# Optimization experiments

Hardware: AMD Instinct MI355X
Metric: run time of the kernel (lower is better)

Reference implementation:

```python
import jax, jax.numpy as jnp
import numpy as np

B, T, C = 2, 2048, 2048
H, KV, D = 16, 4, 128
R = H // KV  # n_rep


def rope_tables(T, D, dtype=jnp.float32):
    half = D // 2
    theta = 1.0 / (10000.0 ** (jnp.arange(half, dtype=jnp.float32) / half))
    pos = jnp.arange(T, dtype=jnp.float32)
    freqs = pos[:, None] * theta[None, :]            # (T, half)
    freqs = jnp.concatenate([freqs, freqs], axis=-1)  # (T, D)
    return jnp.cos(freqs).astype(dtype), jnp.sin(freqs).astype(dtype)


def rotate_half(x):
    half = x.shape[-1] // 2
    return jnp.concatenate([-x[..., half:], x[..., :half]], axis=-1)


def apply_rope(x, cos, sin):
    # x: (B, heads, T, D); cos/sin: (T, D) broadcast over batch/heads
    return x * cos + rotate_half(x) * sin


def setup_inputs() -> dict:
    key = jax.random.key(0)
    kx, kq, kk, kv, ko = jax.random.split(key, 5)
    x = jax.random.normal(kx, (B, T, C), dtype=jnp.float32)
    s = 0.02
    Wq = jax.random.normal(kq, (C, H * D), dtype=jnp.float32) * s
    Wk = jax.random.normal(kk, (C, KV * D), dtype=jnp.float32) * s
    Wv = jax.random.normal(kv, (C, KV * D), dtype=jnp.float32) * s
    Wo = jax.random.normal(ko, (C, C), dtype=jnp.float32) * s
    return {"x": x, "Wq": Wq, "Wk": Wk, "Wv": Wv, "Wo": Wo}


def reference(x, Wq, Wk, Wv, Wo):
    cos, sin = rope_tables(T, D, x.dtype)
    # projections -> (B, heads, T, D)
    q = (x @ Wq).reshape(B, T, H, D).transpose(0, 2, 1, 3)
    k = (x @ Wk).reshape(B, T, KV, D).transpose(0, 2, 1, 3)
    v = (x @ Wv).reshape(B, T, KV, D).transpose(0, 2, 1, 3)
    q = apply_rope(q, cos, sin)
    k = apply_rope(k, cos, sin)
    # GQA: repeat_interleave(n_rep, dim=1) == grouping heads as (KV, R)
    qg = q.reshape(B, KV, R, T, D)
    scale = 1.0 / jnp.sqrt(jnp.asarray(D, dtype=x.dtype))
    scores = jnp.einsum('bgrtd,bgsd->bgrts', qg, k) * scale  # (B,KV,R,T,T)
    causal = jnp.tril(jnp.ones((T, T), dtype=bool))
    scores = jnp.where(causal, scores, jnp.asarray(-jnp.inf, dtype=scores.dtype))
    attn = jax.nn.softmax(scores, axis=-1)
    out = jnp.einsum('bgrts,bgsd->bgrtd', attn, v)            # (B,KV,R,T,D)
    out = out.reshape(B, H, T, D).transpose(0, 2, 1, 3).reshape(B, T, C)
    return out @ Wo
```

## Files before the change

kernel.cpp:

```cpp
#include <hip/hip_runtime.h>
#include <hip/hip_bf16.h>


typedef unsigned short u16;
typedef __attribute__((ext_vector_type(8))) short   bf8_t;
typedef __attribute__((ext_vector_type(4))) float   f4_t;
typedef __attribute__((ext_vector_type(4))) int     i4_t;
typedef __attribute__((ext_vector_type(4))) u16     u16x4;

static constexpr int cB = 2, cT = 2048, cC = 2048, cH = 16, cKV = 4, cD = 128;
static constexpr int cBT = cB * cT;
static constexpr int cNQKV = cH*cD + 2*cKV*cD;
static constexpr int cKOFF = cH*cD;
static constexpr int cVOFF = cH*cD + cKV*cD;
static constexpr float cQSCALE = 0.08838834764831843f;

#define DEVI __device__ __forceinline__

#define AS1G(p) ((const __attribute__((address_space(1))) void*)(unsigned long long)(p))
#define AS3I(x) ((__attribute__((address_space(3))) void*)(unsigned)(x))

DEVI u16 f2b(float f) {
  union { float f; unsigned u; } v; v.f = f;
  unsigned r = v.u + 0x7FFFu + ((v.u >> 16) & 1u);
  return (u16)(r >> 16);
}
DEVI float b2f(u16 h) {
  union { unsigned u; float f; } v; v.u = ((unsigned)h) << 16; return v.f;
}
DEVI f4_t mfma16(bf8_t a, bf8_t b, f4_t c) {
  return __builtin_amdgcn_mfma_f32_16x16x32_bf16(a, b, c, 0, 0, 0);
}


__global__ void k_cvt_x(const float* __restrict__ x, u16* __restrict__ xb) {
  int i = (blockIdx.x * 256 + threadIdx.x) * 4;
  float4 v = *(const float4*)(x + i);
  u16x4 o; o.x = f2b(v.x); o.y = f2b(v.y); o.z = f2b(v.z); o.w = f2b(v.w);
  *(u16x4*)(xb + i) = o;
}

__global__ void k_tconv(const float* __restrict__ s0, int ld0, int ncut0,
                        const float* __restrict__ s1, int ld1, int ncut1,
                        const float* __restrict__ s2, int ld2,
                        u16* __restrict__ dst, int Kdim) {
  __shared__ float tile[64][65];
  int n0 = blockIdx.x * 64, k0 = blockIdx.y * 64;
  int tid = threadIdx.x;
#pragma unroll
  for (int r = 0; r < 16; ++r) {
    int idx = r * 256 + tid;
    int kk = idx >> 6, nn = idx & 63;
    int n = n0 + nn;
    float v;
    if (n < ncut0)      v = s0[(size_t)(k0 + kk) * ld0 + n];
    else if (n < ncut1) v = s1[(size_t)(k0 + kk) * ld1 + (n - ncut0)];
    else                v = s2[(size_t)(k0 + kk) * ld2 + (n - ncut1)];
    tile[kk][nn] = v;
  }
  __syncthreads();
#pragma unroll
  for (int r = 0; r < 16; ++r) {
    int idx = r * 256 + tid;
    int nn = idx >> 6, kk = idx & 63;
    dst[(size_t)(n0 + nn) * Kdim + k0 + kk] = f2b(tile[kk][nn]);
  }
}

__global__ void k_ropetab(float* __restrict__ cosb, float* __restrict__ sinb) {
  int i = blockIdx.x * 256 + threadIdx.x;
  int t = i >> 6, d = i & 63;
  float th = powf(10000.f, -(float)d / 64.f);
  float f = (float)t * th;
  cosb[i] = cosf(f);
  sinb[i] = sinf(f);
}

__global__ void k_rope(u16* __restrict__ qkv, const float* __restrict__ cosb,
                       const float* __restrict__ sinb) {
  int i = blockIdx.x * 256 + threadIdx.x;
  int row = i / 320, p = i - row * 320;
  int head = p >> 4, d4 = (p & 15) << 2;
  int t = row & (cT - 1);
  u16* base = qkv + (size_t)row * cNQKV + head * cD + d4;
  u16x4 lo4 = *(u16x4*)base;
  u16x4 hi4 = *(u16x4*)(base + 64);
  float4 cv = *(const float4*)(cosb + (t << 6) + d4);
  float4 sv = *(const float4*)(sinb + (t << 6) + d4);
  float sc = (head < cH) ? cQSCALE : 1.f;
  u16x4 olo, ohi;
#pragma unroll
  for (int j = 0; j < 4; ++j) {
    float lo = b2f(lo4[j]), hi = b2f(hi4[j]);
    float c = (&cv.x)[j], s = (&sv.x)[j];
    olo[j] = f2b((lo * c - hi * s) * sc);
    ohi[j] = f2b((hi * c + lo * s) * sc);
  }
  *(u16x4*)base = olo;
  *(u16x4*)(base + 64) = ohi;
}

__global__ void k_vtrans(const u16* __restrict__ qkv, u16* __restrict__ vt) {
  __shared__ u16 tile[64][65];
  int s0 = blockIdx.x * 64, d0 = blockIdx.y * 64, bg = blockIdx.z;
  int b = bg >> 2, g = bg & 3;
  int tid = threadIdx.x;
#pragma unroll
  for (int r = 0; r < 16; ++r) {
    int idx = r * 256 + tid;
    int ss = idx >> 6, dd = idx & 63;
    tile[ss][dd] = qkv[(size_t)(b * cT + s0 + ss) * cNQKV + cVOFF + g * cD + d0 + dd];
  }
  __syncthreads();
#pragma unroll
  for (int r = 0; r < 16; ++r) {
    int idx = r * 256 + tid;
    int dd = idx >> 6, ss = idx & 63;
    vt[(size_t)((b * cKV + g) * cD + d0 + dd) * cT + s0 + ss] = tile[ss][dd];
  }
}

template <int N_, bool OUTF32>
__global__ __launch_bounds__(256) void k_gemm_bt(const u16* __restrict__ A,
                                                 const u16* __restrict__ Bt,
                                                 void* __restrict__ Cout) {
  constexpr int K_ = 2048;
  __shared__ __align__(16) u16 As[128 * 32];
  __shared__ __align__(16) u16 Bs[128 * 32];
  int tid = threadIdx.x;
  int l = tid & 63;
  int w = tid >> 6;
  int l15 = l & 15, l4 = l >> 4;
  int wm = w >> 1, wn = w & 1;
  int m0 = blockIdx.y * 128, n0 = blockIdx.x * 128;

  int srow = tid >> 2;
  int kby = (tid & 3) * 16;
  const char* aG = (const char*)A  + ((size_t)(m0 + srow) * K_) * 2 + kby;
  const char* bG = (const char*)Bt + ((size_t)(n0 + srow) * K_) * 2 + kby;
  const size_t rstride = (size_t)64 * K_ * 2;

  unsigned asB = __builtin_amdgcn_readfirstlane(
      (unsigned)(unsigned long long)(const char*)As + (unsigned)w * 1024u);
  unsigned bsB = __builtin_amdgcn_readfirstlane(
      (unsigned)(unsigned long long)(const char*)Bs + (unsigned)w * 1024u);

  f4_t acc[4][4];
  f4_t zf = {0.f, 0.f, 0.f, 0.f};
#pragma unroll
  for (int m = 0; m < 4; ++m)
#pragma unroll
    for (int n = 0; n < 4; ++n) acc[m][n] = zf;

  for (int ks = 0; ks < K_ / 32; ++ks) {
    const char* aN = aG + (size_t)ks * 64;
    const char* bN = bG + (size_t)ks * 64;
    __builtin_amdgcn_global_load_lds(AS1G(aN),            AS3I(asB),        16, 0, 0);
    __builtin_amdgcn_global_load_lds(AS1G(aN + rstride),  AS3I(asB + 4096), 16, 0, 0);
    __builtin_amdgcn_global_load_lds(AS1G(bN),            AS3I(bsB),        16, 0, 0);
    __builtin_amdgcn_global_load_lds(AS1G(bN + rstride),  AS3I(bsB + 4096), 16, 0, 0);
    __syncthreads();

    bf8_t af[4], bfr[4];
#pragma unroll
    for (int m = 0; m < 4; ++m)
      af[m] = *(const bf8_t*)&As[(wm * 64 + m * 16 + l15) * 32 + l4 * 8];
#pragma unroll
    for (int n = 0; n < 4; ++n)
      bfr[n] = *(const bf8_t*)&Bs[(wn * 64 + n * 16 + l15) * 32 + l4 * 8];
#pragma unroll
    for (int m = 0; m < 4; ++m)
#pragma unroll
      for (int n = 0; n < 4; ++n)
        acc[m][n] = mfma16(af[m], bfr[n], acc[m][n]);
    __syncthreads();
  }
#pragma unroll
  for (int m = 0; m < 4; ++m) {
#pragma unroll
    for (int n = 0; n < 4; ++n) {
      int col = n0 + wn * 64 + n * 16 + l15;
#pragma unroll
      for (int r = 0; r < 4; ++r) {
        int row = m0 + wm * 64 + m * 16 + l4 * 4 + r;
        if (OUTF32)
          ((float*)Cout)[(size_t)row * N_ + col] = acc[m][n][r];
        else
          ((u16*)Cout)[(size_t)row * N_ + col] = f2b(acc[m][n][r]);
      }
    }
  }
}

__global__ __launch_bounds__(256) void k_attn(const u16* __restrict__ qkv,
                                              const u16* __restrict__ vt,
                                              u16* __restrict__ obuf) {
  __shared__ __align__(16) u16 Kl[64 * 128];
  __shared__ __align__(16) u16 Vl[128 * 64];
  __shared__ __align__(16) u16 Pl[4][16 * 64];

  int bh = blockIdx.x;
  int qt = 31 - (int)blockIdx.y;
  int b = bh >> 4, h = bh & 15;
  int g = h >> 2;
  int tid = threadIdx.x;
  int l = tid & 63, w = tid >> 6;
  int l15 = l & 15, l4 = l >> 4;

  const char* qkvB = (const char*)qkv;
  const char* vtB  = (const char*)vt;
  const size_t kRowBase = ((size_t)(b * cT) * cNQKV + cKOFF + g * cD) * 2;
  const size_t vRowBase = ((size_t)((b * cKV + g) * cD)) * cT * 2;
  f4_t zf = {0.f, 0.f, 0.f, 0.f};

  int trow = qt * 64 + w * 16 + l15;
  const u16* qrow = qkv + (size_t)(b * cT + trow) * cNQKV + h * cD;
  bf8_t qf[4];
#pragma unroll
  for (int kc = 0; kc < 4; ++kc) qf[kc] = *(const bf8_t*)(qrow + kc * 32 + l4 * 8);

  f4_t occ[8];
#pragma unroll
  for (int c = 0; c < 8; ++c) occ[c] = zf;
  float mrun[4], lrun[4];
#pragma unroll
  for (int r = 0; r < 4; ++r) { mrun[r] = -__builtin_inff(); lrun[r] = 0.f; }

  i4_t kreg[4], vreg[4];
#pragma unroll
  for (int rr = 0; rr < 4; ++rr) {
    int off = tid * 16 + rr * 4096;
    int s = off >> 8, dby = off & 255;
    kreg[rr] = *(const i4_t*)(qkvB + kRowBase + (size_t)s * (cNQKV * 2) + dby);
    int dv = off >> 7, sby = off & 127;
    vreg[rr] = *(const i4_t*)(vtB + vRowBase + (size_t)dv * (cT * 2) + sby);
  }

  int nt = qt + 1;
  for (int it = 0; it < nt; ++it) {
#pragma unroll
    for (int rr = 0; rr < 4; ++rr) {
      int off = tid * 16 + rr * 4096;
      int s = off >> 8, dby = off & 255;
      *(i4_t*)((char*)Kl + (((s << 8) + dby) ^ ((s & 7) << 4))) = kreg[rr];
      int dv = off >> 7, sby = off & 127;
      *(i4_t*)((char*)Vl + (((dv << 7) + sby) ^ ((dv & 7) << 4))) = vreg[rr];
    }
    __syncthreads();
    if (it + 1 < nt) {
      int s0n = (it + 1) * 64;
#pragma unroll
      for (int rr = 0; rr < 4; ++rr) {
        int off = tid * 16 + rr * 4096;
        int s = off >> 8, dby = off & 255;
        kreg[rr] = *(const i4_t*)(qkvB + kRowBase + (size_t)(s0n + s) * (cNQKV * 2) + dby);
        int dv = off >> 7, sby = off & 127;
        vreg[rr] = *(const i4_t*)(vtB + vRowBase + (size_t)dv * (cT * 2) + (size_t)s0n * 2 + sby);
      }
    }
    f4_t sac[4];
#pragma unroll
    for (int ct = 0; ct < 4; ++ct) sac[ct] = zf;
    __builtin_amdgcn_s_setprio(1);
#pragma unroll
    for (int ct = 0; ct < 4; ++ct) {
      int srow = ct * 16 + l15;
#pragma unroll
      for (int kc = 0; kc < 4; ++kc) {
        bf8_t kf = *(const bf8_t*)((const char*)Kl +
                   (((srow << 8) + (kc << 6) + (l4 << 4)) ^ ((srow & 7) << 4)));
        sac[ct] = mfma16(qf[kc], kf, sac[ct]);
      }
    }
    __builtin_amdgcn_s_setprio(0);
    float p[4][4], fac[4];
    if (it < qt) {
#pragma unroll
      for (int r = 0; r < 4; ++r) {
        float mx = fmaxf(fmaxf(sac[0][r], sac[1][r]), fmaxf(sac[2][r], sac[3][r]));
        mx = fmaxf(mx, __shfl_xor(mx, 1));
        mx = fmaxf(mx, __shfl_xor(mx, 2));
        mx = fmaxf(mx, __shfl_xor(mx, 4));
        mx = fmaxf(mx, __shfl_xor(mx, 8));
        float mnew = fmaxf(mrun[r], mx);
        fac[r] = __expf(mrun[r] - mnew);
        mrun[r] = mnew;
        float ps = 0.f;
#pragma unroll
        for (int ct = 0; ct < 4; ++ct) {
          float pv = __expf(sac[ct][r] - mnew);
          p[ct][r] = pv;
          ps += pv;
        }
        ps += __shfl_xor(ps, 1);
        ps += __shfl_xor(ps, 2);
        ps += __shfl_xor(ps, 4);
        ps += __shfl_xor(ps, 8);
        lrun[r] = lrun[r] * fac[r] + ps;
      }
    } else {
      int s0 = it * 64;
#pragma unroll
      for (int r = 0; r < 4; ++r) {
        int tg = qt * 64 + w * 16 + l4 * 4 + r;
        float mx = -__builtin_inff();
#pragma unroll
        for (int ct = 0; ct < 4; ++ct) {
          int sg = s0 + ct * 16 + l15;
          float sv = (sg <= tg) ? sac[ct][r] : -__builtin_inff();
          mx = fmaxf(mx, sv);
        }
        mx = fmaxf(mx, __shfl_xor(mx, 1));
        mx = fmaxf(mx, __shfl_xor(mx, 2));
        mx = fmaxf(mx, __shfl_xor(mx, 4));
        mx = fmaxf(mx, __shfl_xor(mx, 8));
        float mnew = fmaxf(mrun[r], mx);
        fac[r] = __expf(mrun[r] - mnew);
        mrun[r] = mnew;
        float ps = 0.f;
#pragma unroll
        for (int ct = 0; ct < 4; ++ct) {
          int sg = s0 + ct * 16 + l15;
          float pv = (sg <= tg) ? __expf(sac[ct][r] - mnew) : 0.f;
          p[ct][r] = pv;
          ps += pv;
        }
        ps += __shfl_xor(ps, 1);
        ps += __shfl_xor(ps, 2);
        ps += __shfl_xor(ps, 4);
        ps += __shfl_xor(ps, 8);
        lrun[r] = lrun[r] * fac[r] + ps;
      }
    }
#pragma unroll
    for (int c = 0; c < 8; ++c)
#pragma unroll
      for (int r = 0; r < 4; ++r) occ[c][r] *= fac[r];
#pragma unroll
    for (int ct = 0; ct < 4; ++ct)
#pragma unroll
      for (int r = 0; r < 4; ++r) {
        int prow = l4 * 4 + r, pcol = ct * 16 + l15;
        unsigned pby = (unsigned)((prow << 7) + (pcol << 1));
        *(u16*)((char*)&Pl[w][0] + (pby ^ ((prow & 7) << 4))) = f2b(p[ct][r]);
      }
    asm volatile("s_waitcnt lgkmcnt(0)" ::: "memory");
    __builtin_amdgcn_sched_barrier(0);
    __builtin_amdgcn_s_setprio(1);
#pragma unroll
    for (int kc2 = 0; kc2 < 2; ++kc2) {
      unsigned rby = (unsigned)((l15 << 7) + (kc2 << 6) + (l4 << 4));
      bf8_t pf = *(const bf8_t*)((const char*)&Pl[w][0] + (rby ^ ((l15 & 7) << 4)));
#pragma unroll
      for (int c = 0; c < 8; ++c) {
        int drow = c * 16 + l15;
        bf8_t vf = *(const bf8_t*)((const char*)Vl +
                   (((drow << 7) + (kc2 << 6) + (l4 << 4)) ^ ((drow & 7) << 4)));
        occ[c] = mfma16(pf, vf, occ[c]);
      }
    }
    __builtin_amdgcn_s_setprio(0);
    __syncthreads();
  }
  float inv[4];
#pragma unroll
  for (int r = 0; r < 4; ++r) inv[r] = 1.f / lrun[r];
  int orow0 = qt * 64 + w * 16 + l4 * 4;
#pragma unroll
  for (int c = 0; c < 8; ++c) {
    int col = h * cD + c * 16 + l15;
#pragma unroll
    for (int r = 0; r < 4; ++r)
      obuf[(size_t)(b * cT + orow0 + r) * (cH * cD) + col] = f2b(occ[c][r] * inv[r]);
  }
}


extern "C" void kernel_launch(void* const* d_in, const int* in_sizes, int n_in,
                              void* d_out, int out_size, void* d_ws, size_t ws_size,
                              hipStream_t stream) {
  (void)in_sizes; (void)n_in; (void)out_size; (void)ws_size;
  const float* x  = (const float*)d_in[0];
  const float* Wq = (const float*)d_in[1];
  const float* Wk = (const float*)d_in[2];
  const float* Wv = (const float*)d_in[3];
  const float* Wo = (const float*)d_in[4];

  char* p = (char*)d_ws;
  u16* xb   = (u16*)p;  p += (size_t)cBT * cC * 2;
  u16* wt   = (u16*)p;  p += (size_t)cNQKV * cC * 2;
  u16* wot  = (u16*)p;  p += (size_t)cC * cC * 2;
  u16* qkv  = (u16*)p;  p += (size_t)cBT * cNQKV * 2;
  u16* vt   = (u16*)p;  p += (size_t)cB * cKV * cD * cT * 2;
  float* cosb = (float*)p; p += (size_t)cT * 64 * 4;
  float* sinb = (float*)p; p += (size_t)cT * 64 * 4;
  u16* ob = xb;

  k_cvt_x<<<dim3(cBT * cC / 1024), 256, 0, stream>>>(x, xb);
  k_tconv<<<dim3(cNQKV / 64, cC / 64), 256, 0, stream>>>(
      Wq, cH * cD, cH * cD, Wk, cKV * cD, cH * cD + cKV * cD, Wv, cKV * cD, wt, cC);
  k_tconv<<<dim3(cC / 64, cC / 64), 256, 0, stream>>>(
      Wo, cC, cC, Wo, cC, cC, Wo, cC, wot, cC);
  k_ropetab<<<dim3(cT * 64 / 256), 256, 0, stream>>>(cosb, sinb);
  k_gemm_bt<cNQKV, false><<<dim3(cNQKV / 128, cBT / 128), 256, 0, stream>>>(xb, wt, qkv);
  k_rope<<<dim3(cBT * 320 / 256), 256, 0, stream>>>(qkv, cosb, sinb);
  k_vtrans<<<dim3(cT / 64, cD / 64, cB * cKV), 256, 0, stream>>>(qkv, vt);
  k_attn<<<dim3(cB * cH, cT / 64), 256, 0, stream>>>(qkv, vt, ob);
  k_gemm_bt<cC, true><<<dim3(cC / 128, cBT / 128), 256, 0, stream>>>(ob, wot, d_out);
}
```

Baseline: 330.3 us.

## Replace GEMM with 128x256-tile, 4-stage async LDS pipeline and swizzled layout

Replaces the 128x128 single-buffered GEMM with a 512-thread kernel that computes 128x256 output tiles. Global-to-LDS loads are issued three k-steps ahead into a 4-slot ring buffer, gated by explicit vmcnt waits and a single barrier per step, instead of load-then-sync on every step. LDS columns are XOR-swizzled to reduce bank conflicts on the fragment reads. The goal is to hide global memory latency and raise reuse of the B operand, at the cost of more LDS use (96KB) and fewer blocks in the grid.

```diff
diff --git a/kernel.cpp b/kernel.cpp
--- a/kernel.cpp
+++ b/kernel.cpp
@@ -120,30 +120,34 @@
   }
 }
 
-template <int N_, bool OUTF32>
-__global__ __launch_bounds__(256) void k_gemm_bt(const u16* __restrict__ A,
-                                                 const u16* __restrict__ Bt,
-                                                 void* __restrict__ Cout) {
-  constexpr int K_ = 2048;
-  __shared__ __align__(16) u16 As[128 * 32];
-  __shared__ __align__(16) u16 Bs[128 * 32];
-  int tid = threadIdx.x;
-  int l = tid & 63;
-  int w = tid >> 6;
-  int l15 = l & 15, l4 = l >> 4;
-  int wm = w >> 1, wn = w & 1;
-  int m0 = blockIdx.y * 128, n0 = blockIdx.x * 128;
-
-  int srow = tid >> 2;
-  int kby = (tid & 3) * 16;
-  const char* aG = (const char*)A  + ((size_t)(m0 + srow) * K_) * 2 + kby;
-  const char* bG = (const char*)Bt + ((size_t)(n0 + srow) * K_) * 2 + kby;
-  const size_t rstride = (size_t)64 * K_ * 2;
-
-  unsigned asB = __builtin_amdgcn_readfirstlane(
-      (unsigned)(unsigned long long)(const char*)As + (unsigned)w * 1024u);
-  unsigned bsB = __builtin_amdgcn_readfirstlane(
-      (unsigned)(unsigned long long)(const char*)Bs + (unsigned)w * 1024u);
+template <int NBLK, bool OUTF32>
+__global__ __launch_bounds__(512, 2) void k_gemm256(const u16* __restrict__ A,
+                                                    const u16* __restrict__ Bt,
+                                                    void* __restrict__ Cout) {
+  constexpr int K_ = 2048, NT = K_ / 32;
+  __shared__ __align__(16) u16 lds[4 * 12288];
+  const int tid = threadIdx.x;
+  const int l = tid & 63, wid = tid >> 6;
+  const int l15 = l & 15, l4 = l >> 4;
+  const int wr = wid >> 2, wc = wid & 3;
+  const int m0 = blockIdx.y * 128, n0 = blockIdx.x * 256;
+
+  const int rowS = tid >> 2, slotS = tid & 3;
+  const int colS = (slotS * 16) ^ (((rowS >> 1) & 3) << 4);
+  const char* aG  = (const char*)A  + ((size_t)(m0 + rowS) * K_) * 2 + colS;
+  const char* bG0 = (const char*)Bt + ((size_t)(n0 + rowS) * K_) * 2 + colS;
+  const char* bG1 = (const char*)Bt + ((size_t)(n0 + 128 + rowS) * K_) * 2 + colS;
+
+  const unsigned ldsB = (unsigned)(unsigned long long)(const char*)lds;
+  const unsigned aDst  = __builtin_amdgcn_readfirstlane(ldsB + (unsigned)wid * 1024u);
+  const unsigned bDst0 = __builtin_amdgcn_readfirstlane(ldsB + 8192u + (unsigned)wid * 1024u);
+  const unsigned bDst1 = __builtin_amdgcn_readfirstlane(ldsB + 16384u + (unsigned)wid * 1024u);
+
+#define G_STAGE(kt_) { \
+    const unsigned sb_ = (unsigned)((kt_) & 3) * 24576u; \
+    __builtin_amdgcn_global_load_lds(AS1G(aG  + (size_t)(kt_) * 64), AS3I(aDst  + sb_), 16, 0, 0); \
+    __builtin_amdgcn_global_load_lds(AS1G(bG0 + (size_t)(kt_) * 64), AS3I(bDst0 + sb_), 16, 0, 0); \
+    __builtin_amdgcn_global_load_lds(AS1G(bG1 + (size_t)(kt_) * 64), AS3I(bDst1 + sb_), 16, 0, 0); }
 
   f4_t acc[4][4];
   f4_t zf = {0.f, 0.f, 0.f, 0.f};
@@ -152,41 +156,49 @@
 #pragma unroll
     for (int n = 0; n < 4; ++n) acc[m][n] = zf;
 
-  for (int ks = 0; ks < K_ / 32; ++ks) {
-    const char* aN = aG + (size_t)ks * 64;
-    const char* bN = bG + (size_t)ks * 64;
-    __builtin_amdgcn_global_load_lds(AS1G(aN),            AS3I(asB),        16, 0, 0);
-    __builtin_amdgcn_global_load_lds(AS1G(aN + rstride),  AS3I(asB + 4096), 16, 0, 0);
-    __builtin_amdgcn_global_load_lds(AS1G(bN),            AS3I(bsB),        16, 0, 0);
-    __builtin_amdgcn_global_load_lds(AS1G(bN + rstride),  AS3I(bsB + 4096), 16, 0, 0);
-    __syncthreads();
-
-    bf8_t af[4], bfr[4];
+  G_STAGE(0); G_STAGE(1); G_STAGE(2);
+
+  for (int kt = 0; kt < NT; ++kt) {
+    if (kt < NT - 2)       asm volatile("s_waitcnt vmcnt(6)" ::: "memory");
+    else if (kt == NT - 2) asm volatile("s_waitcnt vmcnt(3)" ::: "memory");
+    else                   asm volatile("s_waitcnt vmcnt(0)" ::: "memory");
+    __builtin_amdgcn_s_barrier();
+    __builtin_amdgcn_sched_barrier(0);
+    if (kt + 3 < NT) G_STAGE(kt + 3);
+
+    const unsigned sb = (unsigned)(kt & 3) * 24576u;
+    bf8_t af[4], bf[4];
+#pragma unroll
+    for (int m = 0; m < 4; ++m) {
+      int row = wr * 64 + m * 16 + l15;
+      af[m] = *(const bf8_t*)((const char*)lds + sb + row * 64 +
+                              ((l4 * 16) ^ (((row >> 1) & 3) << 4)));
+    }
+#pragma unroll
+    for (int n = 0; n < 4; ++n) {
+      int row = wc * 64 + n * 16 + l15;
+      bf[n] = *(const bf8_t*)((const char*)lds + sb + 8192 + row * 64 +
+                              ((l4 * 16) ^ (((row >> 1) & 3) << 4)));
+    }
 #pragma unroll
     for (int m = 0; m < 4; ++m)
-      af[m] = *(const bf8_t*)&As[(wm * 64 + m * 16 + l15) * 32 + l4 * 8];
-#pragma unroll
-    for (int n = 0; n < 4; ++n)
-      bfr[n] = *(const bf8_t*)&Bs[(wn * 64 + n * 16 + l15) * 32 + l4 * 8];
-#pragma unroll
-    for (int m = 0; m < 4; ++m)
 #pragma unroll
       for (int n = 0; n < 4; ++n)
-        acc[m][n] = mfma16(af[m], bfr[n], acc[m][n]);
-    __syncthreads();
-  }
+        acc[m][n] = mfma16(af[m], bf[n], acc[m][n]);
+  }
+#undef G_STAGE
 #pragma unroll
   for (int m = 0; m < 4; ++m) {
 #pragma unroll
     for (int n = 0; n < 4; ++n) {
-      int col = n0 + wn * 64 + n * 16 + l15;
+      int col = n0 + wc * 64 + n * 16 + l15;
 #pragma unroll
       for (int r = 0; r < 4; ++r) {
-        int row = m0 + wm * 64 + m * 16 + l4 * 4 + r;
+        int row = m0 + wr * 64 + m * 16 + l4 * 4 + r;
         if (OUTF32)
-          ((float*)Cout)[(size_t)row * N_ + col] = acc[m][n][r];
+          ((float*)Cout)[(size_t)row * NBLK + col] = acc[m][n][r];
         else
-          ((u16*)Cout)[(size_t)row * N_ + col] = f2b(acc[m][n][r]);
+          ((u16*)Cout)[(size_t)row * NBLK + col] = f2b(acc[m][n][r]);
       }
     }
   }
@@ -402,9 +414,9 @@
   k_tconv<<<dim3(cC / 64, cC / 64), 256, 0, stream>>>(
       Wo, cC, cC, Wo, cC, cC, Wo, cC, wot, cC);
   k_ropetab<<<dim3(cT * 64 / 256), 256, 0, stream>>>(cosb, sinb);
-  k_gemm_bt<cNQKV, false><<<dim3(cNQKV / 128, cBT / 128), 256, 0, stream>>>(xb, wt, qkv);
+  k_gemm256<cNQKV, false><<<dim3(cNQKV / 256, cBT / 128), 512, 0, stream>>>(xb, wt, qkv);
   k_rope<<<dim3(cBT * 320 / 256), 256, 0, stream>>>(qkv, cosb, sinb);
   k_vtrans<<<dim3(cT / 64, cD / 64, cB * cKV), 256, 0, stream>>>(qkv, vt);
   k_attn<<<dim3(cB * cH, cT / 64), 256, 0, stream>>>(qkv, vt, ob);
-  k_gemm_bt<cC, true><<<dim3(cC / 128, cBT / 128), 256, 0, stream>>>(ob, wot, d_out);
-}
+  k_gemm256<cC, true><<<dim3(cC / 256, cBT / 128), 512, 0, stream>>>(ob, wot, d_out);
+}
```

Result: no change. 325.0 us (-1.6%).
